# Kernel tuning notes

Measured on AMD Instinct MI355X. Metric: run time of the kernel, lower is better.

## Reference

```python
import jax, jax.numpy as jnp
import numpy as np
from jax import lax

N_WAY, N_SUPPORT, N_QUERY = 16, 256, 512
D_IN, D_EMB = 4096, 1024
N_CLUSTERS, MAX_ITER = 5, 100


def setup_inputs() -> dict:
    key = jax.random.key(0)
    k1, k2, kw, kb = jax.random.split(key, 4)
    support = jax.random.normal(k1, (N_WAY, N_SUPPORT, D_IN), jnp.float32)
    query = jax.random.normal(k2, (N_WAY, N_QUERY, D_IN), jnp.float32)
    W = jax.random.normal(kw, (D_IN, D_EMB), jnp.float32) / np.float32(np.sqrt(D_IN))
    b = jax.random.normal(kb, (D_EMB,), jnp.float32) * 0.01
    return {"support": support, "query": query, "W": W, "b": b}


def _sqdist(x, c):
    # x [n,d], c [k,d] -> [n,k] squared euclidean distances
    return (jnp.sum(x * x, -1, keepdims=True)
            - 2.0 * (x @ c.T)
            + jnp.sum(c * c, -1))


def _kmeans(x, init):
    # x [n,d], init [k,d]; fixed-iteration Lloyd's kmeans (converged state is a
    # fixed point of the update, matching the torch early-break semantics).
    n = x.shape[0]
    ones = jnp.ones((n,), x.dtype)

    def step(c, _):
        assign = jnp.argmin(_sqdist(x, c), axis=1)              # [n]
        sums = jax.ops.segment_sum(x, assign, num_segments=N_CLUSTERS)
        cnt = jax.ops.segment_sum(ones, assign, num_segments=N_CLUSTERS)
        # empty cluster keeps its old centroid
        new_c = jnp.where(cnt[:, None] > 0,
                          sums / jnp.maximum(cnt, 1.0)[:, None], c)
        return new_c, None

    c, _ = lax.scan(step, init, None, length=MAX_ITER)
    return c


def _forward(support, query, W, b):
    # encoder: shared linear over flattened (n_way * n) rows
    s = (support.reshape(-1, D_IN) @ W + b).reshape(N_WAY, N_SUPPORT, D_EMB)
    q = (query.reshape(-1, D_IN) @ W + b).reshape(N_WAY, N_QUERY, D_EMB)

    # per-class kmeans init: random subset of that class's support embeddings
    keys = jax.random.split(jax.random.key(42), N_WAY)

    def init_fn(key, class_emb):
        idx = jax.random.permutation(key, N_SUPPORT)[:N_CLUSTERS]
        return class_emb[idx]

    inits = jax.vmap(init_fn)(keys, s)                 # [n_way, k, d]
    cluster_protos = jax.vmap(_kmeans)(s, inits)       # [n_way, k, d]
    class_protos = cluster_protos.mean(axis=1)         # [n_way, d]

    # cdist(query_emb [b,n,d], protos [c,d]) -> [b,n,c]
    d2 = (jnp.sum(q * q, -1)[..., None]
          - 2.0 * jnp.einsum('bnd,cd->bnc', q, class_protos)
          + jnp.sum(class_protos * class_protos, -1))
    distances = jnp.sqrt(jnp.maximum(d2, 0.0))
    return -distances                                  # logits [n_way, n_query, n_classes]


def reference(support, query, W, b):
    return _forward(support, query, W, b)
```

## Files before the change

### kernel.cpp

```cpp
#include <hip/hip_runtime.h>
#include <cstdint>
#include <cstddef>


typedef __attribute__((ext_vector_type(4))) float f32x4;
typedef __attribute__((ext_vector_type(8))) short s16x8;
typedef __attribute__((ext_vector_type(4))) short s16x4;
typedef __attribute__((ext_vector_type(8))) __bf16 bf16x8;

__device__ __forceinline__ unsigned short f2bf(float f) {
  unsigned u = __float_as_uint(f);
  return (unsigned short)((u + 0x7FFFu + ((u >> 16) & 1u)) >> 16);
}
__device__ __forceinline__ float bf2f(unsigned short h) {
  return __uint_as_float(((unsigned)h) << 16);
}

typedef const __attribute__((address_space(1))) void GV;
typedef __attribute__((address_space(3))) void LV;
__device__ __forceinline__ void gload_lds16(const void* g, void* l) {
  __builtin_amdgcn_global_load_lds((GV*)g, (LV*)l, 16, 0, 0);
}
__device__ __forceinline__ f32x4 mfma16(bf16x8 a, bf16x8 b, f32x4 c) {
  return __builtin_amdgcn_mfma_f32_16x16x32_bf16(a, b, c, 0, 0, 0);
}
__device__ __forceinline__ float wave_sum(float v) {
#pragma unroll
  for (int st = 1; st < 64; st <<= 1) v += __shfl_xor(v, st);
  return v;
}

__device__ __forceinline__ void tf2x32(unsigned k0, unsigned k1, unsigned x0,
                                       unsigned x1, unsigned& y0, unsigned& y1) {
  unsigned ks0 = k0, ks1 = k1, ks2 = k0 ^ k1 ^ 0x1BD11BDAu;
  x0 += ks0; x1 += ks1;
  const int rA[4] = {13, 15, 26, 6};
  const int rB[4] = {17, 29, 16, 24};
#define ROTL(v, d) (((v) << (d)) | ((v) >> (32 - (d))))
#define RG(R)                                     \
  _Pragma("unroll") for (int i = 0; i < 4; i++) { \
    x0 += x1; x1 = ROTL(x1, R[i]); x1 ^= x0;      \
  }
  RG(rA); x0 += ks1; x1 += ks2 + 1u;
  RG(rB); x0 += ks2; x1 += ks0 + 2u;
  RG(rA); x0 += ks0; x1 += ks1 + 3u;
  RG(rB); x0 += ks1; x1 += ks2 + 4u;
  RG(rA); x0 += ks2; x1 += ks0 + 5u;
#undef RG
#undef ROTL
  y0 = x0; y1 = x1;
}

__global__ __launch_bounds__(256) void prepw_k(const float* __restrict__ W,
                                               short* __restrict__ WhiT,
                                               short* __restrict__ WloT) {
  int bk = blockIdx.x, bn = blockIdx.y;
  __shared__ float tile[64][65];
  int t = threadIdx.x;
#pragma unroll
  for (int i = 0; i < 4; i++) {
    int row = i * 16 + (t >> 4);
    int col = (t & 15) * 4;
    f32x4 v = *(const f32x4*)(W + (size_t)(bk * 64 + row) * 1024 + bn * 64 + col);
    tile[row][col + 0] = v[0]; tile[row][col + 1] = v[1];
    tile[row][col + 2] = v[2]; tile[row][col + 3] = v[3];
  }
  __syncthreads();
#pragma unroll
  for (int i = 0; i < 4; i++) {
    int nrow = i * 16 + (t >> 4);
    int kcol = (t & 15) * 4;
    s16x4 hv, lv;
#pragma unroll
    for (int e = 0; e < 4; e++) {
      float v = tile[kcol + e][nrow];
      unsigned short h = f2bf(v);
      float hf = bf2f(h);
      hv[e] = (short)h;
      lv[e] = (short)f2bf(v - hf);
    }
    size_t off = (size_t)(bn * 64 + nrow) * 4096 + bk * 64 + kcol;
    *(s16x4*)(WhiT + off) = hv;
    *(s16x4*)(WloT + off) = lv;
  }
}

__global__ __launch_bounds__(256) void prepa_k(const float* __restrict__ sup,
                                               const float* __restrict__ qry,
                                               short* __restrict__ Shi,
                                               short* __restrict__ Slo,
                                               short* __restrict__ Qhi) {
  size_t gid = (size_t)blockIdx.x * 256 + threadIdx.x;
  const size_t sup_n8 = (size_t)4096 * 4096 / 8;
  if (gid < sup_n8) {
    const float* src = sup + gid * 8;
    f32x4 v0 = *(const f32x4*)src, v1 = *(const f32x4*)(src + 4);
    s16x8 h, l;
#pragma unroll
    for (int e = 0; e < 4; e++) {
      unsigned short hh = f2bf(v0[e]);
      h[e] = (short)hh; l[e] = (short)f2bf(v0[e] - bf2f(hh));
    }
#pragma unroll
    for (int e = 0; e < 4; e++) {
      unsigned short hh = f2bf(v1[e]);
      h[4 + e] = (short)hh; l[4 + e] = (short)f2bf(v1[e] - bf2f(hh));
    }
    *(s16x8*)(Shi + gid * 8) = h;
    *(s16x8*)(Slo + gid * 8) = l;
  } else {
    size_t q = gid - sup_n8;
    const float* src = qry + q * 8;
    f32x4 v0 = *(const f32x4*)src, v1 = *(const f32x4*)(src + 4);
    s16x8 h;
#pragma unroll
    for (int e = 0; e < 4; e++) h[e] = (short)f2bf(v0[e]);
#pragma unroll
    for (int e = 0; e < 4; e++) h[4 + e] = (short)f2bf(v1[e]);
    *(s16x8*)(Qhi + q * 8) = h;
  }
}

__global__ __launch_bounds__(256) void gemm_fast_k(
    const short* __restrict__ Shi, const short* __restrict__ Slo,
    const short* __restrict__ Qhi, const short* __restrict__ WhiT,
    const short* __restrict__ WloT, const float* __restrict__ bias,
    float* __restrict__ emb) {
  __shared__ short lds[4 * 128 * 64];
  short* Ah = lds;
  short* Al = lds + 8192;
  short* Bh = lds + 16384;
  short* Bl = lds + 24576;
  const int bid = blockIdx.x;
  const int bm = bid % 96, bn = bid / 96;
  const bool is_sup = bm < 32;
  const int t = threadIdx.x, lane = t & 63, w = t >> 6;
  const int wr = w >> 1, wc = w & 1;
  const int fr = lane & 15, kg = lane >> 4;
  const short* Ag = is_sup ? (Shi + (size_t)bm * 128 * 4096)
                           : (Qhi + (size_t)(bm - 32) * 128 * 4096);
  const short* Alg = Slo + (size_t)bm * 128 * 4096;
  f32x4 acc[4][4] = {};
  const int ls = lane >> 3;
  const int lc = lane & 7;

  for (int kt = 0; kt < 64; ++kt) {
    const int k0 = kt * 64;
    __syncthreads();
#pragma unroll
    for (int j = 0; j < 4; j++) {
      int rowl = w * 32 + j * 8 + ls;
      int cch = (lc ^ (ls & 7)) * 8;
      size_t aoff = (size_t)rowl * 4096 + k0 + cch;
      size_t boff = (size_t)(bn * 128 + rowl) * 4096 + k0 + cch;
      int ldst = (w * 32 + j * 8) * 64;
      gload_lds16(Ag + aoff, Ah + ldst);
      gload_lds16(WhiT + boff, Bh + ldst);
      if (is_sup) {
        gload_lds16(Alg + aoff, Al + ldst);
        gload_lds16(WloT + boff, Bl + ldst);
      }
    }
    __syncthreads();
#pragma unroll
    for (int ks = 0; ks < 2; ++ks) {
      const int cx = ((ks * 4 + kg) ^ (fr & 7)) * 8;
      bf16x8 ahf[4], bhf[4];
#pragma unroll
      for (int mi = 0; mi < 4; mi++) {
        int arow = wr * 64 + mi * 16 + fr;
        ahf[mi] = __builtin_bit_cast(bf16x8, *(const s16x8*)(Ah + arow * 64 + cx));
      }
#pragma unroll
      for (int ni = 0; ni < 4; ni++) {
        int brow = wc * 64 + ni * 16 + fr;
        bhf[ni] = __builtin_bit_cast(bf16x8, *(const s16x8*)(Bh + brow * 64 + cx));
      }
      if (is_sup) {
        bf16x8 alf[4], blf[4];
#pragma unroll
        for (int mi = 0; mi < 4; mi++) {
          int arow = wr * 64 + mi * 16 + fr;
          alf[mi] =
              __builtin_bit_cast(bf16x8, *(const s16x8*)(Al + arow * 64 + cx));
        }
#pragma unroll
        for (int ni = 0; ni < 4; ni++) {
          int brow = wc * 64 + ni * 16 + fr;
          blf[ni] =
              __builtin_bit_cast(bf16x8, *(const s16x8*)(Bl + brow * 64 + cx));
        }
#pragma unroll
        for (int mi = 0; mi < 4; mi++)
#pragma unroll
          for (int ni = 0; ni < 4; ni++) {
            acc[mi][ni] = mfma16(ahf[mi], bhf[ni], acc[mi][ni]);
            acc[mi][ni] = mfma16(ahf[mi], blf[ni], acc[mi][ni]);
            acc[mi][ni] = mfma16(alf[mi], bhf[ni], acc[mi][ni]);
          }
      } else {
#pragma unroll
        for (int mi = 0; mi < 4; mi++)
#pragma unroll
          for (int ni = 0; ni < 4; ni++)
            acc[mi][ni] = mfma16(ahf[mi], bhf[ni], acc[mi][ni]);
      }
    }
  }
#pragma unroll
  for (int ni = 0; ni < 4; ni++) {
    int gc = bn * 128 + wc * 64 + ni * 16 + fr;
    float bv = bias[gc];
#pragma unroll
    for (int mi = 0; mi < 4; mi++) {
      int gr = bm * 128 + wr * 64 + mi * 16 + kg * 4;
#pragma unroll
      for (int r = 0; r < 4; r++)
        emb[(size_t)(gr + r) * 1024 + gc] = acc[mi][ni][r] + bv;
    }
  }
}

__global__ __launch_bounds__(256) void gemm_all_k(
    const float* __restrict__ sup, const float* __restrict__ qry,
    const short* __restrict__ WhiT, const short* __restrict__ WloT,
    const float* __restrict__ bias, float* __restrict__ emb) {
  __shared__ short lds[4 * 128 * 64];
  short* Ah = lds;
  short* Al = lds + 8192;
  short* Bh = lds + 16384;
  short* Bl = lds + 24576;
  const int bid = blockIdx.x;
  const int bm = bid % 96, bn = bid / 96;
  const bool is_sup = bm < 32;
  const int t = threadIdx.x, lane = t & 63, w = t >> 6;
  const int wr = w >> 1, wc = w & 1;
  const int fr = lane & 15, kg = lane >> 4;
  const float* Abase = is_sup ? (sup + (size_t)bm * 128 * 4096)
                              : (qry + (size_t)(bm - 32) * 128 * 4096);
  f32x4 acc[4][4] = {};
  const int ls = lane >> 3, lc = lane & 7;

  for (int kt = 0; kt < 64; ++kt) {
    const int k0 = kt * 64;
    __syncthreads();
#pragma unroll
    for (int i = 0; i < 4; i++) {
      int row = i * 32 + w * 8 + ls;
      const float* src = Abase + (size_t)row * 4096 + k0 + lc * 8;
      f32x4 v0 = *(const f32x4*)src;
      f32x4 v1 = *(const f32x4*)(src + 4);
      s16x8 hs;
#pragma unroll
      for (int e = 0; e < 4; e++) hs[e] = (short)f2bf(v0[e]);
#pragma unroll
      for (int e = 0; e < 4; e++) hs[4 + e] = (short)f2bf(v1[e]);
      int chunk = lc ^ (row & 7);
      *(s16x8*)(Ah + row * 64 + chunk * 8) = hs;
      if (is_sup) {
        s16x8 lsv;
#pragma unroll
        for (int e = 0; e < 4; e++)
          lsv[e] = (short)f2bf(v0[e] - bf2f((unsigned short)hs[e]));
#pragma unroll
        for (int e = 0; e < 4; e++)
          lsv[4 + e] = (short)f2bf(v1[e] - bf2f((unsigned short)hs[4 + e]));
        *(s16x8*)(Al + row * 64 + chunk * 8) = lsv;
      }
    }
#pragma unroll
    for (int j = 0; j < 4; j++) {
      int rowl = w * 32 + j * 8 + ls;
      int cch = (lc ^ (ls & 7)) * 8;
      size_t goff = (size_t)(bn * 128 + rowl) * 4096 + k0 + cch;
      gload_lds16(WhiT + goff, Bh + (w * 32 + j * 8) * 64);
      if (is_sup) gload_lds16(WloT + goff, Bl + (w * 32 + j * 8) * 64);
    }
    __syncthreads();
#pragma unroll
    for (int ks = 0; ks < 2; ++ks) {
      const int cx = ((ks * 4 + kg) ^ (fr & 7)) * 8;
      bf16x8 ahf[4], bhf[4];
#pragma unroll
      for (int mi = 0; mi < 4; mi++) {
        int arow = wr * 64 + mi * 16 + fr;
        ahf[mi] = __builtin_bit_cast(bf16x8, *(const s16x8*)(Ah + arow * 64 + cx));
      }
#pragma unroll
      for (int ni = 0; ni < 4; ni++) {
        int brow = wc * 64 + ni * 16 + fr;
        bhf[ni] = __builtin_bit_cast(bf16x8, *(const s16x8*)(Bh + brow * 64 + cx));
      }
      if (is_sup) {
        bf16x8 alf[4], blf[4];
#pragma unroll
        for (int mi = 0; mi < 4; mi++) {
          int arow = wr * 64 + mi * 16 + fr;
          alf[mi] =
              __builtin_bit_cast(bf16x8, *(const s16x8*)(Al + arow * 64 + cx));
        }
#pragma unroll
        for (int ni = 0; ni < 4; ni++) {
          int brow = wc * 64 + ni * 16 + fr;
          blf[ni] =
              __builtin_bit_cast(bf16x8, *(const s16x8*)(Bl + brow * 64 + cx));
        }
#pragma unroll
        for (int mi = 0; mi < 4; mi++)
#pragma unroll
          for (int ni = 0; ni < 4; ni++) {
            acc[mi][ni] = mfma16(ahf[mi], bhf[ni], acc[mi][ni]);
            acc[mi][ni] = mfma16(ahf[mi], blf[ni], acc[mi][ni]);
            acc[mi][ni] = mfma16(alf[mi], bhf[ni], acc[mi][ni]);
          }
      } else {
#pragma unroll
        for (int mi = 0; mi < 4; mi++)
#pragma unroll
          for (int ni = 0; ni < 4; ni++)
            acc[mi][ni] = mfma16(ahf[mi], bhf[ni], acc[mi][ni]);
      }
    }
  }
#pragma unroll
  for (int ni = 0; ni < 4; ni++) {
    int gc = bn * 128 + wc * 64 + ni * 16 + fr;
    float bv = bias[gc];
#pragma unroll
    for (int mi = 0; mi < 4; mi++) {
      int gr = bm * 128 + wr * 64 + mi * 16 + kg * 4;
#pragma unroll
      for (int r = 0; r < 4; r++)
        emb[(size_t)(gr + r) * 1024 + gc] = acc[mi][ni][r] + bv;
    }
  }
}

__global__ __launch_bounds__(256) void gram_k(const float* __restrict__ emb,
                                              float* __restrict__ G) {
  int c = blockIdx.x >> 4, tl = blockIdx.x & 15, ti = tl >> 2, tj = tl & 3;
  __shared__ float As[64][36];
  __shared__ float Bs[32][68];
  int t = threadIdx.x, ty = t >> 4, tx = t & 15;
  const float* base = emb + (size_t)c * 256 * 1024;
  float acc[4][4] = {};
  for (int k0 = 0; k0 < 1024; k0 += 32) {
    __syncthreads();
    {
      int r = t >> 2, seg = t & 3;
      const float* pa = base + (size_t)(ti * 64 + r) * 1024 + k0 + seg * 8;
      f32x4 va0 = *(const f32x4*)pa, va1 = *(const f32x4*)(pa + 4);
      *(f32x4*)(&As[r][seg * 8]) = va0;
      *(f32x4*)(&As[r][seg * 8 + 4]) = va1;
      const float* pb = base + (size_t)(tj * 64 + r) * 1024 + k0 + seg * 8;
      f32x4 vb0 = *(const f32x4*)pb, vb1 = *(const f32x4*)(pb + 4);
#pragma unroll
      for (int e = 0; e < 4; e++) Bs[seg * 8 + e][r] = vb0[e];
#pragma unroll
      for (int e = 0; e < 4; e++) Bs[seg * 8 + 4 + e][r] = vb1[e];
    }
    __syncthreads();
#pragma unroll 4
    for (int kk = 0; kk < 32; kk++) {
      float a0 = As[ty * 4 + 0][kk], a1 = As[ty * 4 + 1][kk];
      float a2 = As[ty * 4 + 2][kk], a3 = As[ty * 4 + 3][kk];
      f32x4 bv = *(const f32x4*)(&Bs[kk][tx * 4]);
#pragma unroll
      for (int jdx = 0; jdx < 4; jdx++) {
        acc[0][jdx] = fmaf(a0, bv[jdx], acc[0][jdx]);
        acc[1][jdx] = fmaf(a1, bv[jdx], acc[1][jdx]);
        acc[2][jdx] = fmaf(a2, bv[jdx], acc[2][jdx]);
        acc[3][jdx] = fmaf(a3, bv[jdx], acc[3][jdx]);
      }
    }
  }
#pragma unroll
  for (int i = 0; i < 4; i++) {
    int gr = ti * 64 + ty * 4 + i;
#pragma unroll
    for (int j = 0; j < 4; j++)
      G[(size_t)c * 65536 + (size_t)gr * 256 + tj * 64 + tx * 4 + j] = acc[i][j];
  }
}

__global__ __launch_bounds__(256) void diag_k(const float* __restrict__ emb,
                                              float* __restrict__ G) {
  int r = blockIdx.x * 4 + (threadIdx.x >> 6);
  int lane = threadIdx.x & 63;
  const float* x = emb + (size_t)r * 1024;
  double acc = 0.0;
#pragma unroll
  for (int ch = 0; ch < 16; ch++) {
    float v = x[ch * 64 + lane];
    acc = fma((double)v, (double)v, acc);
  }
#pragma unroll
  for (int st = 1; st < 64; st <<= 1) acc += __shfl_xor(acc, st);
  if (lane == 0) {
    int c = r >> 8, i = r & 255;
    G[(size_t)c * 65536 + (size_t)i * 256 + i] = (float)acc;
  }
}

__global__ __launch_bounds__(256) void kmeans2_k(const float* __restrict__ G,
                                                 float* __restrict__ wts) {
  const int c = blockIdx.x;
  const int t = threadIdx.x, lane = t & 63, w = t >> 6;
  __shared__ unsigned dmL[256], nmL[256];
  __shared__ unsigned short chg[256];
  __shared__ unsigned sk[256];
  __shared__ unsigned idx5[5];
  __shared__ float Tpart[4][5], Tu[5], C2[5], Minv[5];
  __shared__ int Hp[4][5], Ncnt[5], cntW[4];

  {
    unsigned o0, o1, s0k, s1k, y0, y1;
    tf2x32(0u, 42u, 0u, (unsigned)c, o0, o1);
    tf2x32(o0, o1, 0u, 1u, s0k, s1k);
    tf2x32(s0k, s1k, 0u, (unsigned)t, y0, y1);
    sk[t] = y0 ^ y1;
  }
  __syncthreads();
  {
    unsigned kt_ = sk[t];
    int rank = 0;
    for (int j = 0; j < 256; j++) {
      unsigned kj = sk[j];
      rank += (kj < kt_ || (kj == kt_ && j < t)) ? 1 : 0;
    }
    if (rank < 5) idx5[rank] = (unsigned)t;
  }
  if (t < 5) Minv[t] = 1.0f;
  __syncthreads();

  unsigned m = 0;
#pragma unroll
  for (int k = 0; k < 5; k++) m |= (idx5[k] == (unsigned)t) ? (1u << k) : 0u;

  const float* Gc = G + (size_t)c * 65536;
  float s0 = Gc[(size_t)idx5[0] * 256 + t];
  float s1 = Gc[(size_t)idx5[1] * 256 + t];
  float s2 = Gc[(size_t)idx5[2] * 256 + t];
  float s3 = Gc[(size_t)idx5[3] * 256 + t];
  float s4 = Gc[(size_t)idx5[4] * 256 + t];

  for (int it = 0; it < 100; ++it) {
    float v0 = (m & 1u) ? s0 : 0.0f;
    float v1 = (m & 2u) ? s1 : 0.0f;
    float v2 = (m & 4u) ? s2 : 0.0f;
    float v3 = (m & 8u) ? s3 : 0.0f;
    float v4 = (m & 16u) ? s4 : 0.0f;
#pragma unroll
    for (int st = 1; st < 64; st <<= 1) {
      v0 += __shfl_xor(v0, st); v1 += __shfl_xor(v1, st);
      v2 += __shfl_xor(v2, st); v3 += __shfl_xor(v3, st);
      v4 += __shfl_xor(v4, st);
    }
    if (lane == 0) {
      Tpart[w][0] = v0; Tpart[w][1] = v1; Tpart[w][2] = v2;
      Tpart[w][3] = v3; Tpart[w][4] = v4;
    }
    __syncthreads();
    if (t < 5) {
      float T = Tpart[0][t] + Tpart[1][t] + Tpart[2][t] + Tpart[3][t];
      float iv = Minv[t];
      Tu[t] = T * iv * iv;
      C2[t] = -2.0f * iv;
    }
    __syncthreads();
    float d0 = fmaf(C2[0], s0, Tu[0]);
    float d1 = fmaf(C2[1], s1, Tu[1]);
    float d2 = fmaf(C2[2], s2, Tu[2]);
    float d3 = fmaf(C2[3], s3, Tu[3]);
    float d4 = fmaf(C2[4], s4, Tu[4]);
    int a_t = 0;
    float dmn = d0;
    if (d1 < dmn) { dmn = d1; a_t = 1; }
    if (d2 < dmn) { dmn = d2; a_t = 2; }
    if (d3 < dmn) { dmn = d3; a_t = 3; }
    if (d4 < dmn) { dmn = d4; a_t = 4; }
#pragma unroll
    for (int k = 0; k < 5; k++) {
      unsigned long long bal = __ballot(a_t == k);
      if (lane == 0) Hp[w][k] = (int)__popcll(bal);
    }
    __syncthreads();
    if (t < 5) Ncnt[t] = Hp[0][t] + Hp[1][t] + Hp[2][t] + Hp[3][t];
    __syncthreads();
    unsigned nm = 0;
#pragma unroll
    for (int k = 0; k < 5; k++) {
      int bit = (Ncnt[k] > 0) ? (a_t == k ? 1 : 0) : (int)((m >> k) & 1u);
      nm |= ((unsigned)bit) << k;
    }
    unsigned dmb = nm ^ m;
    unsigned long long bal = __ballot(dmb != 0);
    int myrank = (int)__popcll(bal & ((1ull << lane) - 1ull));
    if (lane == 0) cntW[w] = (int)__popcll(bal);
    nmL[t] = nm; dmL[t] = dmb;
    __syncthreads();
    int base = 0, ntot = 0;
#pragma unroll
    for (int ww = 0; ww < 4; ww++) {
      int cw = cntW[ww];
      if (ww < w) base += cw;
      ntot += cw;
    }
    if (ntot == 0) break;
    if (dmb != 0) chg[base + myrank] = (unsigned short)t;
    m = nm;
    if (t < 5 && Ncnt[t] > 0) Minv[t] = 1.0f / (float)Ncnt[t];
    __syncthreads();
    for (int p = 0; p < ntot; p += 4) {
      float g[4]; int jj[4];
#pragma unroll
      for (int q = 0; q < 4; q++) {
        int idx = p + q;
        jj[q] = (idx < ntot) ? (int)chg[idx] : -1;
        g[q] = (jj[q] >= 0) ? Gc[(size_t)jj[q] * 256 + t] : 0.0f;
      }
#pragma unroll
      for (int q = 0; q < 4; q++) {
        if (jj[q] < 0) continue;
        unsigned db = dmL[jj[q]], nb = nmL[jj[q]];
        float gv = g[q];
        if (db & 1u)  s0 += (nb & 1u)  ? gv : -gv;
        if (db & 2u)  s1 += (nb & 2u)  ? gv : -gv;
        if (db & 4u)  s2 += (nb & 4u)  ? gv : -gv;
        if (db & 8u)  s3 += (nb & 8u)  ? gv : -gv;
        if (db & 16u) s4 += (nb & 16u) ? gv : -gv;
      }
    }
    __syncthreads();
  }
  float wv = 0.0f;
#pragma unroll
  for (int k = 0; k < 5; k++)
    if ((m >> k) & 1u) wv += 0.2f * Minv[k];
  wts[c * 256 + t] = wv;
}

__global__ __launch_bounds__(256) void proto_k(const float* __restrict__ emb,
                                               const float* __restrict__ wts,
                                               float* __restrict__ protos) {
  int c = blockIdx.x, t = threadIdx.x;
  __shared__ float wl[256];
  wl[t] = wts[c * 256 + t];
  __syncthreads();
  f32x4 acc = {};
  const float* base = emb + (size_t)c * 256 * 1024 + t * 4;
  for (int j = 0; j < 256; j++) {
    f32x4 v = *(const f32x4*)(base + (size_t)j * 1024);
    float wj = wl[j];
#pragma unroll
    for (int e = 0; e < 4; e++) acc[e] = fmaf(wj, v[e], acc[e]);
  }
  *(f32x4*)(protos + (size_t)c * 1024 + t * 4) = acc;
}

__global__ __launch_bounds__(256) void dist_k(const float* __restrict__ emb,
                                              const float* __restrict__ protos,
                                              float* __restrict__ out) {
  __shared__ float P[16 * 1024];
  int t = threadIdx.x, lane = t & 63, w = t >> 6;
#pragma unroll
  for (int i = 0; i < 16; i++) {
    int off = i * 1024 + t * 4;
    *(f32x4*)(P + off) = *(const f32x4*)(protos + off);
  }
  __syncthreads();
  float psq_keep = 0.0f;
  for (int p = 0; p < 16; p++) {
    float partial = 0.0f;
#pragma unroll
    for (int ch = 0; ch < 16; ch++) {
      float x = P[p * 1024 + ch * 64 + lane];
      partial = fmaf(x, x, partial);
    }
    partial = wave_sum(partial);
    if (lane == p) psq_keep = partial;
  }
  const float* qbase = emb + (size_t)4096 * 1024;
  int r0 = blockIdx.x * 16 + w * 4;
  for (int ri = 0; ri < 4; ri++) {
    int row = r0 + ri;
    const float* q = qbase + (size_t)row * 1024;
    float qv[16];
#pragma unroll
    for (int ch = 0; ch < 16; ch++) qv[ch] = q[ch * 64 + lane];
    float qsq = 0.0f;
#pragma unroll
    for (int ch = 0; ch < 16; ch++) qsq = fmaf(qv[ch], qv[ch], qsq);
    qsq = wave_sum(qsq);
    float dsel = 0.0f;
    for (int p = 0; p < 16; p++) {
      float dp = 0.0f;
#pragma unroll
      for (int ch = 0; ch < 16; ch++)
        dp = fmaf(qv[ch], P[p * 1024 + ch * 64 + lane], dp);
      dp = wave_sum(dp);
      if (lane == p) dsel = dp;
    }
    if (lane < 16) {
      float d2 = qsq - 2.0f * dsel + psq_keep;
      d2 = fmaxf(d2, 0.0f);
      out[(size_t)row * 16 + lane] = -sqrtf(d2);
    }
  }
}

extern "C" void kernel_launch(void* const* d_in, const int* in_sizes, int n_in,
                              void* d_out, int out_size, void* d_ws,
                              size_t ws_size, hipStream_t stream) {
  const float* sup = (const float*)d_in[0];
  const float* qry = (const float*)d_in[1];
  const float* W = (const float*)d_in[2];
  const float* b = (const float*)d_in[3];
  float* out = (float*)d_out;
  char* ws = (char*)d_ws;
  (void)in_sizes; (void)n_in; (void)out_size;

  const size_t NEED_FAST = 205602816ULL;
  if (ws_size >= NEED_FAST) {
    short* WhiT = (short*)(ws + 0);
    short* WloT = (short*)(ws + 8388608);
    short* Shi = (short*)(ws + 16777216);
    short* Slo = (short*)(ws + 50331648);
    short* Qhi = (short*)(ws + 83886080);
    float* emb = (float*)(ws + 150994944);
    float* G = (float*)(ws + 201326592);
    float* wts = (float*)(ws + 205520896);
    float* protos = (float*)(ws + 205537280);

    prepw_k<<<dim3(64, 16), 256, 0, stream>>>(W, WhiT, WloT);
    prepa_k<<<24576, 256, 0, stream>>>(sup, qry, Shi, Slo, Qhi);
    gemm_fast_k<<<768, 256, 0, stream>>>(Shi, Slo, Qhi, WhiT, WloT, b, emb);
    gram_k<<<256, 256, 0, stream>>>(emb, G);
    diag_k<<<1024, 256, 0, stream>>>(emb, G);
    kmeans2_k<<<16, 256, 0, stream>>>(G, wts);
    proto_k<<<16, 256, 0, stream>>>(emb, wts, protos);
    dist_k<<<512, 256, 0, stream>>>(emb, protos, out);
  } else {
    short* WhiT = (short*)(ws + 0);
    short* WloT = (short*)(ws + 8388608);
    float* emb = (float*)(ws + 16777216);
    float* G = (float*)(ws + 67108864);
    float* wts = (float*)(ws + 71303168);
    float* protos = (float*)(ws + 71319552);

    prepw_k<<<dim3(64, 16), 256, 0, stream>>>(W, WhiT, WloT);
    gemm_all_k<<<768, 256, 0, stream>>>(sup, qry, WhiT, WloT, b, emb);
    gram_k<<<256, 256, 0, stream>>>(emb, G);
    diag_k<<<1024, 256, 0, stream>>>(emb, G);
    kmeans2_k<<<16, 256, 0, stream>>>(G, wts);
    proto_k<<<16, 256, 0, stream>>>(emb, wts, protos);
    dist_k<<<512, 256, 0, stream>>>(emb, protos, out);
  }
}
```

Before: 501.7 us.

## Split GEMM into support/query kernels, merge prep kernels, parallelize prototype reduction

Merges the W and activation bf16 split-prep kernels into a single launch. The mixed GEMM, which gave support tiles three MFMAs and query tiles one, becomes two kernels: the support kernel uses 64-row tiles over 512 blocks to spread its heavier 3-pass work evenly, and the query kernel is a plain one-pass bf16 GEMM. The 16-block prototype reduction becomes a 256-block partial sum followed by a small final reduction. This costs one extra launch and workspace for the partials, and the support kernel's smaller tiles reuse less data per block.

```diff
diff --git a/kernel.cpp b/kernel.cpp
--- a/kernel.cpp
+++ b/kernel.cpp
@@ -51,115 +51,181 @@
   y0 = x0; y1 = x1;
 }
 
-__global__ __launch_bounds__(256) void prepw_k(const float* __restrict__ W,
-                                               short* __restrict__ WhiT,
-                                               short* __restrict__ WloT) {
-  int bk = blockIdx.x, bn = blockIdx.y;
+__global__ __launch_bounds__(256) void prep_k(
+    const float* __restrict__ W, const float* __restrict__ sup,
+    const float* __restrict__ qry, short* __restrict__ WhiT,
+    short* __restrict__ WloT, short* __restrict__ Shi,
+    short* __restrict__ Slo, short* __restrict__ Qhi) {
   __shared__ float tile[64][65];
   int t = threadIdx.x;
-#pragma unroll
-  for (int i = 0; i < 4; i++) {
-    int row = i * 16 + (t >> 4);
-    int col = (t & 15) * 4;
-    f32x4 v = *(const f32x4*)(W + (size_t)(bk * 64 + row) * 1024 + bn * 64 + col);
-    tile[row][col + 0] = v[0]; tile[row][col + 1] = v[1];
-    tile[row][col + 2] = v[2]; tile[row][col + 3] = v[3];
-  }
-  __syncthreads();
-#pragma unroll
-  for (int i = 0; i < 4; i++) {
-    int nrow = i * 16 + (t >> 4);
-    int kcol = (t & 15) * 4;
-    s16x4 hv, lv;
-#pragma unroll
-    for (int e = 0; e < 4; e++) {
-      float v = tile[kcol + e][nrow];
-      unsigned short h = f2bf(v);
-      float hf = bf2f(h);
-      hv[e] = (short)h;
-      lv[e] = (short)f2bf(v - hf);
-    }
-    size_t off = (size_t)(bn * 64 + nrow) * 4096 + bk * 64 + kcol;
-    *(s16x4*)(WhiT + off) = hv;
-    *(s16x4*)(WloT + off) = lv;
-  }
-}
-
-__global__ __launch_bounds__(256) void prepa_k(const float* __restrict__ sup,
-                                               const float* __restrict__ qry,
-                                               short* __restrict__ Shi,
-                                               short* __restrict__ Slo,
-                                               short* __restrict__ Qhi) {
-  size_t gid = (size_t)blockIdx.x * 256 + threadIdx.x;
-  const size_t sup_n8 = (size_t)4096 * 4096 / 8;
-  if (gid < sup_n8) {
-    const float* src = sup + gid * 8;
-    f32x4 v0 = *(const f32x4*)src, v1 = *(const f32x4*)(src + 4);
-    s16x8 h, l;
-#pragma unroll
-    for (int e = 0; e < 4; e++) {
-      unsigned short hh = f2bf(v0[e]);
-      h[e] = (short)hh; l[e] = (short)f2bf(v0[e] - bf2f(hh));
-    }
-#pragma unroll
-    for (int e = 0; e < 4; e++) {
-      unsigned short hh = f2bf(v1[e]);
-      h[4 + e] = (short)hh; l[4 + e] = (short)f2bf(v1[e] - bf2f(hh));
-    }
-    *(s16x8*)(Shi + gid * 8) = h;
-    *(s16x8*)(Slo + gid * 8) = l;
+  if (blockIdx.x < 1024) {
+    int bk = blockIdx.x & 63, bn = blockIdx.x >> 6;
+#pragma unroll
+    for (int i = 0; i < 4; i++) {
+      int row = i * 16 + (t >> 4);
+      int col = (t & 15) * 4;
+      f32x4 v =
+          *(const f32x4*)(W + (size_t)(bk * 64 + row) * 1024 + bn * 64 + col);
+      tile[row][col + 0] = v[0]; tile[row][col + 1] = v[1];
+      tile[row][col + 2] = v[2]; tile[row][col + 3] = v[3];
+    }
+    __syncthreads();
+#pragma unroll
+    for (int i = 0; i < 4; i++) {
+      int nrow = i * 16 + (t >> 4);
+      int kcol = (t & 15) * 4;
+      s16x4 hv, lv;
+#pragma unroll
+      for (int e = 0; e < 4; e++) {
+        float v = tile[kcol + e][nrow];
+        unsigned short h = f2bf(v);
+        hv[e] = (short)h;
+        lv[e] = (short)f2bf(v - bf2f(h));
+      }
+      size_t off = (size_t)(bn * 64 + nrow) * 4096 + bk * 64 + kcol;
+      *(s16x4*)(WhiT + off) = hv;
+      *(s16x4*)(WloT + off) = lv;
+    }
   } else {
-    size_t q = gid - sup_n8;
-    const float* src = qry + q * 8;
-    f32x4 v0 = *(const f32x4*)src, v1 = *(const f32x4*)(src + 4);
-    s16x8 h;
-#pragma unroll
-    for (int e = 0; e < 4; e++) h[e] = (short)f2bf(v0[e]);
-#pragma unroll
-    for (int e = 0; e < 4; e++) h[4 + e] = (short)f2bf(v1[e]);
-    *(s16x8*)(Qhi + q * 8) = h;
-  }
-}
-
-__global__ __launch_bounds__(256) void gemm_fast_k(
+    size_t gid = (size_t)(blockIdx.x - 1024) * 256 + t;
+    const size_t sup_n8 = (size_t)4096 * 4096 / 8;
+    if (gid < sup_n8) {
+      const float* src = sup + gid * 8;
+      f32x4 v0 = *(const f32x4*)src, v1 = *(const f32x4*)(src + 4);
+      s16x8 h, l;
+#pragma unroll
+      for (int e = 0; e < 4; e++) {
+        unsigned short hh = f2bf(v0[e]);
+        h[e] = (short)hh; l[e] = (short)f2bf(v0[e] - bf2f(hh));
+      }
+#pragma unroll
+      for (int e = 0; e < 4; e++) {
+        unsigned short hh = f2bf(v1[e]);
+        h[4 + e] = (short)hh; l[4 + e] = (short)f2bf(v1[e] - bf2f(hh));
+      }
+      *(s16x8*)(Shi + gid * 8) = h;
+      *(s16x8*)(Slo + gid * 8) = l;
+    } else {
+      size_t q = gid - sup_n8;
+      const float* src = qry + q * 8;
+      f32x4 v0 = *(const f32x4*)src, v1 = *(const f32x4*)(src + 4);
+      s16x8 h;
+#pragma unroll
+      for (int e = 0; e < 4; e++) h[e] = (short)f2bf(v0[e]);
+#pragma unroll
+      for (int e = 0; e < 4; e++) h[4 + e] = (short)f2bf(v1[e]);
+      *(s16x8*)(Qhi + q * 8) = h;
+    }
+  }
+}
+
+__global__ __launch_bounds__(256) void gemm_sup_k(
     const short* __restrict__ Shi, const short* __restrict__ Slo,
-    const short* __restrict__ Qhi, const short* __restrict__ WhiT,
-    const short* __restrict__ WloT, const float* __restrict__ bias,
-    float* __restrict__ emb) {
-  __shared__ short lds[4 * 128 * 64];
+    const short* __restrict__ WhiT, const short* __restrict__ WloT,
+    const float* __restrict__ bias, float* __restrict__ emb) {
+  __shared__ short lds[24576];
   short* Ah = lds;
-  short* Al = lds + 8192;
-  short* Bh = lds + 16384;
-  short* Bl = lds + 24576;
+  short* Al = lds + 4096;
+  short* Bh = lds + 8192;
+  short* Bl = lds + 16384;
   const int bid = blockIdx.x;
-  const int bm = bid % 96, bn = bid / 96;
-  const bool is_sup = bm < 32;
+  const int bm = bid & 63, bn = bid >> 6;
   const int t = threadIdx.x, lane = t & 63, w = t >> 6;
   const int wr = w >> 1, wc = w & 1;
   const int fr = lane & 15, kg = lane >> 4;
-  const short* Ag = is_sup ? (Shi + (size_t)bm * 128 * 4096)
-                           : (Qhi + (size_t)(bm - 32) * 128 * 4096);
-  const short* Alg = Slo + (size_t)bm * 128 * 4096;
-  f32x4 acc[4][4] = {};
-  const int ls = lane >> 3;
-  const int lc = lane & 7;
+  const int ls = lane >> 3, lc = lane & 7;
+  const short* Ag = Shi + (size_t)bm * 64 * 4096;
+  const short* Alg = Slo + (size_t)bm * 64 * 4096;
+  f32x4 acc[2][4] = {};
 
   for (int kt = 0; kt < 64; ++kt) {
     const int k0 = kt * 64;
     __syncthreads();
+    const int cch = (lc ^ ls) * 8;
+#pragma unroll
+    for (int j = 0; j < 2; j++) {
+      int rowl = w * 16 + j * 8 + ls;
+      size_t aoff = (size_t)rowl * 4096 + k0 + cch;
+      int ldst = (w * 16 + j * 8) * 64;
+      gload_lds16(Ag + aoff, Ah + ldst);
+      gload_lds16(Alg + aoff, Al + ldst);
+    }
 #pragma unroll
     for (int j = 0; j < 4; j++) {
       int rowl = w * 32 + j * 8 + ls;
-      int cch = (lc ^ (ls & 7)) * 8;
+      size_t boff = (size_t)(bn * 128 + rowl) * 4096 + k0 + cch;
+      int ldst = (w * 32 + j * 8) * 64;
+      gload_lds16(WhiT + boff, Bh + ldst);
+      gload_lds16(WloT + boff, Bl + ldst);
+    }
+    __syncthreads();
+#pragma unroll
+    for (int ks = 0; ks < 2; ++ks) {
+      const int cx = ((ks * 4 + kg) ^ (fr & 7)) * 8;
+      bf16x8 ahf[2], alf[2], bhf[4], blf[4];
+#pragma unroll
+      for (int mi = 0; mi < 2; mi++) {
+        int arow = wr * 32 + mi * 16 + fr;
+        ahf[mi] = __builtin_bit_cast(bf16x8, *(const s16x8*)(Ah + arow * 64 + cx));
+        alf[mi] = __builtin_bit_cast(bf16x8, *(const s16x8*)(Al + arow * 64 + cx));
+      }
+#pragma unroll
+      for (int ni = 0; ni < 4; ni++) {
+        int brow = wc * 64 + ni * 16 + fr;
+        bhf[ni] = __builtin_bit_cast(bf16x8, *(const s16x8*)(Bh + brow * 64 + cx));
+        blf[ni] = __builtin_bit_cast(bf16x8, *(const s16x8*)(Bl + brow * 64 + cx));
+      }
+#pragma unroll
+      for (int mi = 0; mi < 2; mi++)
+#pragma unroll
+        for (int ni = 0; ni < 4; ni++) {
+          acc[mi][ni] = mfma16(ahf[mi], bhf[ni], acc[mi][ni]);
+          acc[mi][ni] = mfma16(ahf[mi], blf[ni], acc[mi][ni]);
+          acc[mi][ni] = mfma16(alf[mi], bhf[ni], acc[mi][ni]);
+        }
+    }
+  }
+#pragma unroll
+  for (int ni = 0; ni < 4; ni++) {
+    int gc = bn * 128 + wc * 64 + ni * 16 + fr;
+    float bv = bias[gc];
+#pragma unroll
+    for (int mi = 0; mi < 2; mi++) {
+      int gr = bm * 64 + wr * 32 + mi * 16 + kg * 4;
+#pragma unroll
+      for (int r = 0; r < 4; r++)
+        emb[(size_t)(gr + r) * 1024 + gc] = acc[mi][ni][r] + bv;
+    }
+  }
+}
+
+__global__ __launch_bounds__(256) void gemm_qry_k(
+    const short* __restrict__ Qhi, const short* __restrict__ WhiT,
+    const float* __restrict__ bias, float* __restrict__ emb) {
+  __shared__ short lds[16384];
+  short* Ah = lds;
+  short* Bh = lds + 8192;
+  const int bid = blockIdx.x;
+  const int bm = bid & 63, bn = bid >> 6;
+  const int t = threadIdx.x, lane = t & 63, w = t >> 6;
+  const int wr = w >> 1, wc = w & 1;
+  const int fr = lane & 15, kg = lane >> 4;
+  const int ls = lane >> 3, lc = lane & 7;
+  const short* Ag = Qhi + (size_t)bm * 128 * 4096;
+  f32x4 acc[4][4] = {};
+
+  for (int kt = 0; kt < 64; ++kt) {
+    const int k0 = kt * 64;
+    __syncthreads();
+    const int cch = (lc ^ ls) * 8;
+#pragma unroll
+    for (int j = 0; j < 4; j++) {
+      int rowl = w * 32 + j * 8 + ls;
       size_t aoff = (size_t)rowl * 4096 + k0 + cch;
       size_t boff = (size_t)(bn * 128 + rowl) * 4096 + k0 + cch;
       int ldst = (w * 32 + j * 8) * 64;
       gload_lds16(Ag + aoff, Ah + ldst);
       gload_lds16(WhiT + boff, Bh + ldst);
-      if (is_sup) {
-        gload_lds16(Alg + aoff, Al + ldst);
-        gload_lds16(WloT + boff, Bl + ldst);
-      }
     }
     __syncthreads();
 #pragma unroll
@@ -176,35 +242,11 @@
         int brow = wc * 64 + ni * 16 + fr;
         bhf[ni] = __builtin_bit_cast(bf16x8, *(const s16x8*)(Bh + brow * 64 + cx));
       }
-      if (is_sup) {
-        bf16x8 alf[4], blf[4];
-#pragma unroll
-        for (int mi = 0; mi < 4; mi++) {
-          int arow = wr * 64 + mi * 16 + fr;
-          alf[mi] =
-              __builtin_bit_cast(bf16x8, *(const s16x8*)(Al + arow * 64 + cx));
-        }
-#pragma unroll
-        for (int ni = 0; ni < 4; ni++) {
-          int brow = wc * 64 + ni * 16 + fr;
-          blf[ni] =
-              __builtin_bit_cast(bf16x8, *(const s16x8*)(Bl + brow * 64 + cx));
-        }
-#pragma unroll
-        for (int mi = 0; mi < 4; mi++)
-#pragma unroll
-          for (int ni = 0; ni < 4; ni++) {
-            acc[mi][ni] = mfma16(ahf[mi], bhf[ni], acc[mi][ni]);
-            acc[mi][ni] = mfma16(ahf[mi], blf[ni], acc[mi][ni]);
-            acc[mi][ni] = mfma16(alf[mi], bhf[ni], acc[mi][ni]);
-          }
-      } else {
-#pragma unroll
-        for (int mi = 0; mi < 4; mi++)
-#pragma unroll
-          for (int ni = 0; ni < 4; ni++)
-            acc[mi][ni] = mfma16(ahf[mi], bhf[ni], acc[mi][ni]);
-      }
+#pragma unroll
+      for (int mi = 0; mi < 4; mi++)
+#pragma unroll
+        for (int ni = 0; ni < 4; ni++)
+          acc[mi][ni] = mfma16(ahf[mi], bhf[ni], acc[mi][ni]);
     }
   }
 #pragma unroll
@@ -213,7 +255,7 @@
     float bv = bias[gc];
 #pragma unroll
     for (int mi = 0; mi < 4; mi++) {
-      int gr = bm * 128 + wr * 64 + mi * 16 + kg * 4;
+      int gr = 4096 + bm * 128 + wr * 64 + mi * 16 + kg * 4;
 #pragma unroll
       for (int r = 0; r < 4; r++)
         emb[(size_t)(gr + r) * 1024 + gc] = acc[mi][ni][r] + bv;
@@ -540,6 +582,38 @@
   wts[c * 256 + t] = wv;
 }
 
+__global__ __launch_bounds__(256) void proto1_k(const float* __restrict__ emb,
+                                                const float* __restrict__ wts,
+                                                float* __restrict__ part) {
+  int c = blockIdx.x & 15, seg = blockIdx.x >> 4, t = threadIdx.x;
+  __shared__ float wl[16];
+  if (t < 16) wl[t] = wts[c * 256 + seg * 16 + t];
+  __syncthreads();
+  f32x4 acc = {};
+  const float* base = emb + (size_t)(c * 256 + seg * 16) * 1024 + t * 4;
+#pragma unroll
+  for (int j = 0; j < 16; j++) {
+    f32x4 v = *(const f32x4*)(base + (size_t)j * 1024);
+    float wj = wl[j];
+#pragma unroll
+    for (int e = 0; e < 4; e++) acc[e] = fmaf(wj, v[e], acc[e]);
+  }
+  *(f32x4*)(part + ((size_t)seg * 16 + c) * 1024 + t * 4) = acc;
+}
+
+__global__ __launch_bounds__(256) void proto2_k(const float* __restrict__ part,
+                                                float* __restrict__ protos) {
+  int c = blockIdx.x, t = threadIdx.x;
+  f32x4 acc = {};
+#pragma unroll
+  for (int seg = 0; seg < 16; seg++) {
+    f32x4 v = *(const f32x4*)(part + ((size_t)seg * 16 + c) * 1024 + t * 4);
+#pragma unroll
+    for (int e = 0; e < 4; e++) acc[e] += v[e];
+  }
+  *(f32x4*)(protos + (size_t)c * 1024 + t * 4) = acc;
+}
+
 __global__ __launch_bounds__(256) void proto_k(const float* __restrict__ emb,
                                                const float* __restrict__ wts,
                                                float* __restrict__ protos) {
@@ -620,7 +694,7 @@
   char* ws = (char*)d_ws;
   (void)in_sizes; (void)n_in; (void)out_size;
 
-  const size_t NEED_FAST = 205602816ULL;
+  const size_t NEED_FAST = 206651392ULL;
   if (ws_size >= NEED_FAST) {
     short* WhiT = (short*)(ws + 0);
     short* WloT = (short*)(ws + 8388608);
@@ -631,14 +705,16 @@
     float* G = (float*)(ws + 201326592);
     float* wts = (float*)(ws + 205520896);
     float* protos = (float*)(ws + 205537280);
-
-    prepw_k<<<dim3(64, 16), 256, 0, stream>>>(W, WhiT, WloT);
-    prepa_k<<<24576, 256, 0, stream>>>(sup, qry, Shi, Slo, Qhi);
-    gemm_fast_k<<<768, 256, 0, stream>>>(Shi, Slo, Qhi, WhiT, WloT, b, emb);
+    float* part = (float*)(ws + 205602816);
+
+    prep_k<<<25600, 256, 0, stream>>>(W, sup, qry, WhiT, WloT, Shi, Slo, Qhi);
+    gemm_sup_k<<<512, 256, 0, stream>>>(Shi, Slo, WhiT, WloT, b, emb);
+    gemm_qry_k<<<512, 256, 0, stream>>>(Qhi, WhiT, b, emb);
     gram_k<<<256, 256, 0, stream>>>(emb, G);
     diag_k<<<1024, 256, 0, stream>>>(emb, G);
     kmeans2_k<<<16, 256, 0, stream>>>(G, wts);
-    proto_k<<<16, 256, 0, stream>>>(emb, wts, protos);
+    proto1_k<<<256, 256, 0, stream>>>(emb, wts, part);
+    proto2_k<<<16, 256, 0, stream>>>(part, protos);
     dist_k<<<512, 256, 0, stream>>>(emb, protos, out);
   } else {
     short* WhiT = (short*)(ws + 0);
@@ -648,7 +724,8 @@
     float* wts = (float*)(ws + 71303168);
     float* protos = (float*)(ws + 71319552);
 
-    prepw_k<<<dim3(64, 16), 256, 0, stream>>>(W, WhiT, WloT);
+    prep_k<<<1024, 256, 0, stream>>>(W, sup, qry, WhiT, WloT, (short*)0,
+                                     (short*)0, (short*)0);
     gemm_all_k<<<768, 256, 0, stream>>>(sup, qry, WhiT, WloT, b, emb);
     gram_k<<<256, 256, 0, stream>>>(emb, G);
     diag_k<<<1024, 256, 0, stream>>>(emb, G);
```

Result: faster. 444.0 us (-11.5%).
